# Performance work log

Hardware: AMD Instinct MI355X
Metric: run time of the kernel (lower is better)

The kernel has to match this reference:

```python
import jax, jax.numpy as jnp
import numpy as np

B, C, D, H, W_, CT = 2, 64, 12, 20, 40, 32


def setup_inputs() -> dict:
    key = jax.random.key(0)
    ks = jax.random.split(key, 8)
    def w(k, o, i):
        return jax.random.normal(k, (o, i), jnp.float32) / np.float32(np.sqrt(i))
    return dict(
        x=jax.random.normal(ks[0], (B, C, D, H, W_), jnp.float32),
        preds=jax.random.normal(ks[1], (B, D, H, W_), jnp.float32),
        Wq1=w(ks[2], CT, C), Wq2=w(ks[3], CT, CT),
        Wk1=w(ks[4], CT, C), Wk2=w(ks[5], CT, CT),
        Wv=w(ks[6], CT, C), Wo=w(ks[7], C, CT),
    )


def conv_bn_relu(x, Wm, eps=1e-5):
    # 1x1x1 Conv3d (no bias) + BatchNorm3d (batch stats, no affine) + ReLU
    y = jnp.einsum('bcdhw,oc->bodhw', x, Wm)
    mu = y.mean(axis=(0, 2, 3, 4), keepdims=True)
    var = y.var(axis=(0, 2, 3, 4), keepdims=True)
    return jax.nn.relu((y - mu) * jax.lax.rsqrt(var + eps))


def semantic_gather(x, preds):
    # Vectorized equivalent of the nested batch/disp-class loops:
    # per-pixel argmax over disparity planes, softmax within each argmax group,
    # scatter weighted feature into a dense (b, hw, d, c) tensor (zeros elsewhere).
    b, c, d, h, w = x.shape
    p = jax.nn.softmax(preds, axis=1).reshape(b, d, h * w).transpose(0, 2, 1)  # (b,hw,d)
    f = x.reshape(b, c, d, h * w).transpose(0, 3, 2, 1)                        # (b,hw,d,c)
    a = jnp.argmax(p, axis=-1)                                                 # (b,hw) segment ids
    pv = jnp.take_along_axis(p, a[..., None], axis=-1)[..., 0]                 # (b,hw) gathered prob

    def seg_softmax(vals, segs):
        # softmax over pixels sharing the same argmax disparity class
        m = jax.lax.stop_gradient(jax.ops.segment_max(vals, segs, num_segments=d))
        e = jnp.exp(vals - m[segs])
        s = jax.ops.segment_sum(e, segs, num_segments=d)
        return e / s[segs]

    wt = jax.vmap(seg_softmax)(pv, a)                                          # (b,hw)
    fg = jnp.take_along_axis(f, a[:, :, None, None], axis=2)[:, :, 0, :]       # (b,hw,c)
    oh = jax.nn.one_hot(a, d, dtype=x.dtype)                                   # (b,hw,d)
    feats_sl = oh[..., None] * (fg * wt[..., None])[:, :, None, :]             # (b,hw,d,c)
    return feats_sl.reshape(b, h, w, d, c).transpose(0, 4, 3, 1, 2)            # (b,c,d,h,w)


def reference(x, preds, Wq1, Wq2, Wk1, Wk2, Wv, Wo):
    feats_sl = semantic_gather(x, preds)
    key_feats = feats_sl + x
    # SelfAttentionBlock: query/key = 2 conv-bn-relu, value/out = 1 conv-bn-relu
    q = conv_bn_relu(conv_bn_relu(x, Wq1), Wq2)
    k = conv_bn_relu(conv_bn_relu(key_feats, Wk1), Wk2)
    v = conv_bn_relu(key_feats, Wv)
    b, ct, d, h, w = q.shape
    n = d * h * w
    qf = q.reshape(b, ct, n).transpose(0, 2, 1)   # (b,n,ct)
    kf = k.reshape(b, ct, n)                      # (b,ct,n)
    vf = v.reshape(b, ct, n).transpose(0, 2, 1)   # (b,n,ct)
    sim = jnp.einsum('bnc,bcm->bnm', qf, kf) * (ct ** -0.5)
    sim = jax.nn.softmax(sim, axis=-1)
    ctx = jnp.einsum('bnm,bmc->bnc', sim, vf).transpose(0, 2, 1).reshape(b, ct, d, h, w)
    return conv_bn_relu(ctx, Wo)
```

## Files before the change

kernel.cpp:

```cpp
#include <hip/hip_runtime.h>

#define NB 2
#define CIN 64
#define DD 12
#define HWP 800
#define NPOS 9600
#define CT 32
#define QKSCALE 0.25506601f
#define CSH 11.541560327f

typedef __attribute__((ext_vector_type(8))) short short8;
typedef __attribute__((ext_vector_type(16))) float f32x16;

__device__ __forceinline__ ushort f2bf(float x){
    union { float f; unsigned u; } v; v.f = x;
    unsigned r = v.u + 0x7fffu + ((v.u >> 16) & 1u);
    return (ushort)(r >> 16);
}

__global__ __launch_bounds__(256) void seg_kernel(const float* __restrict__ preds,
                                                  int* __restrict__ a, float* __restrict__ wt)
{
    int b = blockIdx.x / DD, seg = blockIdx.x % DD;
    __shared__ float lpv[HWP];
    __shared__ int   la[HWP];
    __shared__ float red[256];
    int t = threadIdx.x;
    for (int i=t; i<HWP; i+=256){
        const float* p = preds + (size_t)b*DD*HWP + i;
        float mx = -INFINITY; int am = 0;
        #pragma unroll
        for (int d=0; d<DD; ++d){ float v = p[d*HWP]; if (v > mx){ mx=v; am=d; } }
        float s = 0.f;
        #pragma unroll
        for (int d=0; d<DD; ++d) s += __expf(p[d*HWP]-mx);
        lpv[i] = 1.f/s; la[i] = am;
        if (seg == 0) a[b*HWP+i] = am;
    }
    __syncthreads();
    float mx = -INFINITY;
    for (int i=t; i<HWP; i+=256) if (la[i]==seg) mx = fmaxf(mx, lpv[i]);
    red[t]=mx; __syncthreads();
    for (int s=128; s>0; s>>=1){ if (t<s) red[t]=fmaxf(red[t],red[t+s]); __syncthreads(); }
    float m = red[0]; __syncthreads();
    if (m == -INFINITY) return;
    float sm = 0.f;
    for (int i=t; i<HWP; i+=256) if (la[i]==seg) sm += __expf(lpv[i]-m);
    red[t]=sm; __syncthreads();
    for (int s=128; s>0; s>>=1){ if (t<s) red[t]+=red[t+s]; __syncthreads(); }
    float ssum = red[0];
    for (int i=t; i<HWP; i+=256) if (la[i]==seg) wt[b*HWP+i] = __expf(lpv[i]-m)/ssum;
}

__global__ __launch_bounds__(256) void conv1_kernel(const float* __restrict__ x,
    const int* __restrict__ a, const float* __restrict__ wt,
    const float* __restrict__ Wq1, const float* __restrict__ Wk1, const float* __restrict__ Wv,
    float* __restrict__ q1, float* __restrict__ k1, float* __restrict__ v1,
    float* __restrict__ part)
{
    __shared__ float lw[6144];
    for (int i=threadIdx.x; i<2048; i+=256){ lw[i]=Wq1[i]; lw[2048+i]=Wk1[i]; lw[4096+i]=Wv[i]; }
    __syncthreads();
    int t = threadIdx.x;
    int posIdx = blockIdx.x*32 + (t&31);
    int g = t>>5;
    int b = posIdx / NPOS, pos = posIdx % NPOS;
    int d = pos / HWP, pix = pos % HWP;
    float fac = 1.f;
    if (a[b*HWP+pix] == d) fac += wt[b*HWP+pix];
    float acc[12];
    #pragma unroll
    for (int j=0;j<12;++j) acc[j]=0.f;
    const float* xb = x + (size_t)b*CIN*NPOS + pos;
    int chBase = g*12;
    for (int c=0;c<CIN;++c){
        float xv = xb[(size_t)c*NPOS];
        const float* wrow = &lw[chBase*64 + c];
        #pragma unroll
        for (int j=0;j<12;++j) acc[j] += xv * wrow[j*64];
    }
    #pragma unroll
    for (int j=0;j<12;++j){
        int ch = chBase + j;
        float val = acc[j];
        if (ch >= 32) val *= fac;
        acc[j] = val;
        if (ch < 32)       q1[((size_t)b*CT + ch)*NPOS + pos] = val;
        else if (ch < 64)  k1[((size_t)b*CT + (ch-32))*NPOS + pos] = val;
        else               v1[((size_t)b*CT + (ch-64))*NPOS + pos] = val;
    }
    #pragma unroll
    for (int j=0;j<12;++j){
        float s = acc[j], qs = acc[j]*acc[j];
        #pragma unroll
        for (int off=16; off; off>>=1){ s += __shfl_xor(s,off); qs += __shfl_xor(qs,off); }
        if ((t&31)==0){
            int ch = chBase+j;
            part[((size_t)ch*600 + blockIdx.x)*2]   = s;
            part[((size_t)ch*600 + blockIdx.x)*2+1] = qs;
        }
    }
}

__global__ __launch_bounds__(64) void statsfin_kernel(const float* __restrict__ part,
    float* __restrict__ mu, float* __restrict__ rs, int nblk)
{
    int ch = blockIdx.x;
    float s=0.f, q=0.f;
    for (int i=threadIdx.x; i<nblk; i+=64){
        s += part[((size_t)ch*nblk+i)*2];
        q += part[((size_t)ch*nblk+i)*2+1];
    }
    #pragma unroll
    for (int off=32; off; off>>=1){ s += __shfl_xor(s,off); q += __shfl_xor(q,off); }
    if (threadIdx.x==0){
        float m = s/19200.f;
        mu[ch]=m; rs[ch]=rsqrtf(q/19200.f - m*m + 1e-5f);
    }
}

__global__ __launch_bounds__(256) void conv2_kernel(const float* __restrict__ q1, const float* __restrict__ k1,
    const float* __restrict__ Wq2, const float* __restrict__ Wk2,
    const float* __restrict__ mu1, const float* __restrict__ rs1,
    float* __restrict__ q2, float* __restrict__ k2, float* __restrict__ part)
{
    __shared__ float lw[2048];
    for (int i=threadIdx.x; i<1024; i+=256){ lw[i]=Wq2[i]; lw[1024+i]=Wk2[i]; }
    __syncthreads();
    int t = threadIdx.x;
    int posIdx = blockIdx.x*32 + (t&31);
    int g = t>>5;
    int b = posIdx / NPOS, pos = posIdx % NPOS;
    const float* src = (g<4) ? q1 : k1;
    const float* wb  = (g<4) ? lw : (lw+1024);
    float* dst       = (g<4) ? q2 : k2;
    int so = (g<4) ? 0 : 32;
    int chBase = (g&3)*8;
    float acc[8];
    #pragma unroll
    for (int j=0;j<8;++j) acc[j]=0.f;
    for (int c=0;c<32;++c){
        float v = src[((size_t)b*CT + c)*NPOS + pos];
        float vn = fmaxf((v - mu1[so+c])*rs1[so+c], 0.f);
        const float* wrow = &wb[chBase*32 + c];
        #pragma unroll
        for (int j=0;j<8;++j) acc[j] += vn * wrow[j*32];
    }
    #pragma unroll
    for (int j=0;j<8;++j)
        dst[((size_t)b*CT + chBase + j)*NPOS + pos] = acc[j];
    #pragma unroll
    for (int j=0;j<8;++j){
        float s = acc[j], qs = acc[j]*acc[j];
        #pragma unroll
        for (int off=16; off; off>>=1){ s += __shfl_xor(s,off); qs += __shfl_xor(qs,off); }
        if ((t&31)==0){
            int ch = so + chBase + j;
            part[((size_t)ch*600 + blockIdx.x)*2]   = s;
            part[((size_t)ch*600 + blockIdx.x)*2+1] = qs;
        }
    }
}

__global__ __launch_bounds__(256) void pack_kernel(const float* __restrict__ q2, const float* __restrict__ k2,
    const float* __restrict__ v1,
    const float* __restrict__ mu2, const float* __restrict__ rs2,
    const float* __restrict__ muv, const float* __restrict__ rsv,
    ushort* __restrict__ Qbf, ushort* __restrict__ KP, ushort* __restrict__ VP)
{
    if (blockIdx.x < 75){
        int idx = blockIdx.x*256 + threadIdx.x;
        int b = idx / NPOS, pos = idx - b*NPOS;
        const float* qsrc = q2 + (size_t)b*CT*NPOS + pos;
        const float* ksrc = k2 + (size_t)b*CT*NPOS + pos;
        unsigned qw[16], kw[16];
        #pragma unroll
        for (int c2=0; c2<16; ++c2){
            int c0 = 2*c2, c1 = 2*c2+1;
            float a0 = fmaxf((qsrc[(size_t)c0*NPOS] - mu2[c0])*rs2[c0], 0.f)*QKSCALE;
            float a1 = fmaxf((qsrc[(size_t)c1*NPOS] - mu2[c1])*rs2[c1], 0.f)*QKSCALE;
            qw[c2] = (unsigned)f2bf(a0) | ((unsigned)f2bf(a1)<<16);
            float b0 = fmaxf((ksrc[(size_t)c0*NPOS] - mu2[32+c0])*rs2[32+c0], 0.f);
            float b1 = fmaxf((ksrc[(size_t)c1*NPOS] - mu2[32+c1])*rs2[32+c1], 0.f);
            kw[c2] = (unsigned)f2bf(b0) | ((unsigned)f2bf(b1)<<16);
        }
        uint4* qd = (uint4*)(Qbf + (size_t)idx*CT);
        #pragma unroll
        for (int j=0;j<4;++j)
            qd[j] = make_uint4(qw[4*j], qw[4*j+1], qw[4*j+2], qw[4*j+3]);
        int kb = pos >> 5, c = pos & 31;
        ushort* base = KP + ((size_t)(b*300 + kb))*1024;
        *(uint4*)(base + (c)*8)          = make_uint4(kw[0],kw[1],kw[2],kw[3]);
        *(uint4*)(base + (c+32)*8)       = make_uint4(kw[4],kw[5],kw[6],kw[7]);
        *(uint4*)(base + 512 + (c)*8)    = make_uint4(kw[8],kw[9],kw[10],kw[11]);
        *(uint4*)(base + 512 + (c+32)*8) = make_uint4(kw[12],kw[13],kw[14],kw[15]);
    } else {
        int idx = (blockIdx.x-75)*256 + threadIdx.x;
        int b = idx / 38400;
        int r = idx - b*38400;
        int c = r / 1200;
        int g8 = r - c*1200;
        int key = g8*8;
        int kb = g8 >> 2, q8 = g8 & 3;
        int p = q8 >> 1, hh = q8 & 1;
        const float* vs = v1 + ((size_t)b*CT + c)*NPOS + key;
        float m = muv[c], rr = rsv[c];
        unsigned wds[4];
        #pragma unroll
        for (int j=0;j<4;++j){
            float a0 = fmaxf((vs[2*j]   - m)*rr, 0.f);
            float a1 = fmaxf((vs[2*j+1] - m)*rr, 0.f);
            wds[j] = (unsigned)f2bf(a0) | ((unsigned)f2bf(a1)<<16);
        }
        *(uint4*)(VP + ((size_t)(b*300 + kb))*1024 + p*512 + (c + 32*hh)*8)
            = make_uint4(wds[0],wds[1],wds[2],wds[3]);
    }
}

__global__ __launch_bounds__(256) void attn_kernel(const ushort* __restrict__ Qbf,
    const ushort* __restrict__ KP, const ushort* __restrict__ VP,
    float* __restrict__ pacc, float* __restrict__ plsum)
{
    __shared__ float mrg[3][64][34];
    int blk = blockIdx.x;
    int b = blk / 450;
    int u = blk - b*450;
    int qb = u % 150, third = u / 150;
    int q0 = qb*64;
    int t = threadIdx.x, wv = t>>6, l = t&63;
    int c = l & 31, h = l >> 5;

    const char* QbU = (const char*)(Qbf + (size_t)b*NPOS*CT);
    const char* KPb = (const char*)KP;
    const char* VPb = (const char*)VP;

    union U { uint4 u; short8 s; };
    U qf0, qf1, qf2, qf3;
    qf0.u = *(const uint4*)(QbU + (((q0 + c)*CT + 8*h)<<1));
    qf1.u = *(const uint4*)(QbU + (((q0 + c)*CT + 16 + 8*h)<<1));
    qf2.u = *(const uint4*)(QbU + (((q0 + 32 + c)*CT + 8*h)<<1));
    qf3.u = *(const uint4*)(QbU + (((q0 + 32 + c)*CT + 16 + 8*h)<<1));

    U ones; ones.u = make_uint4(0x3F803F80u,0x3F803F80u,0x3F803F80u,0x3F803F80u);

    f32x16 acc0, acc1, accl0, accl1, cinit;
    #pragma unroll
    for (int r=0;r<16;++r){ acc0[r]=0.f; acc1[r]=0.f; accl0[r]=0.f; accl1[r]=0.f; cinit[r]=-CSH; }

    unsigned voff = (unsigned)(l*16);
    unsigned ko = (unsigned)(b*300 + third*100 + wv*25)*2048u;

    U nk0,nk1,nv0,nv1;
    nk0.u = *(const uint4*)(KPb + ko + voff);
    nk1.u = *(const uint4*)(KPb + ko + voff + 1024);
    nv0.u = *(const uint4*)(VPb + ko + voff);
    nv1.u = *(const uint4*)(VPb + ko + voff + 1024);

    for (int ck=0; ck<25; ++ck){
        U ka0=nk0, ka1=nk1, va0=nv0, va1=nv1;
        ko += (ck<24) ? 2048u : 0u;
        nk0.u = *(const uint4*)(KPb + ko + voff);
        nk1.u = *(const uint4*)(KPb + ko + voff + 1024);
        nv0.u = *(const uint4*)(VPb + ko + voff);
        nv1.u = *(const uint4*)(VPb + ko + voff + 1024);

        {
            f32x16 s = __builtin_amdgcn_mfma_f32_32x32x16_bf16(ka0.s, qf0.s, cinit,0,0,0);
            s = __builtin_amdgcn_mfma_f32_32x32x16_bf16(ka1.s, qf1.s, s, 0,0,0);
            float p[16];
            #pragma unroll
            for (int r=0;r<16;++r) asm("v_exp_f32 %0, %1" : "=v"(p[r]) : "v"(s[r]));
            unsigned E0,E1,E2,E3,E4,E5,E6,E7;
            asm("v_cvt_pk_bf16_f32 %0,%1,%2" : "=v"(E0) : "v"(p[0]),  "v"(p[1]));
            asm("v_cvt_pk_bf16_f32 %0,%1,%2" : "=v"(E1) : "v"(p[2]),  "v"(p[3]));
            asm("v_cvt_pk_bf16_f32 %0,%1,%2" : "=v"(E2) : "v"(p[4]),  "v"(p[5]));
            asm("v_cvt_pk_bf16_f32 %0,%1,%2" : "=v"(E3) : "v"(p[6]),  "v"(p[7]));
            asm("v_cvt_pk_bf16_f32 %0,%1,%2" : "=v"(E4) : "v"(p[8]),  "v"(p[9]));
            asm("v_cvt_pk_bf16_f32 %0,%1,%2" : "=v"(E5) : "v"(p[10]), "v"(p[11]));
            asm("v_cvt_pk_bf16_f32 %0,%1,%2" : "=v"(E6) : "v"(p[12]), "v"(p[13]));
            asm("v_cvt_pk_bf16_f32 %0,%1,%2" : "=v"(E7) : "v"(p[14]), "v"(p[15]));
            asm("v_permlane32_swap_b32 %0, %1" : "+v"(E0), "+v"(E2));
            asm("v_permlane32_swap_b32 %0, %1" : "+v"(E1), "+v"(E3));
            asm("v_permlane32_swap_b32 %0, %1" : "+v"(E4), "+v"(E6));
            asm("v_permlane32_swap_b32 %0, %1" : "+v"(E5), "+v"(E7));
            U pf1, pf2;
            pf1.u = make_uint4(E0,E1,E2,E3);
            pf2.u = make_uint4(E4,E5,E6,E7);
            acc0  = __builtin_amdgcn_mfma_f32_32x32x16_bf16(va0.s,  pf1.s, acc0, 0,0,0);
            accl0 = __builtin_amdgcn_mfma_f32_32x32x16_bf16(ones.s, pf1.s, accl0,0,0,0);
            acc0  = __builtin_amdgcn_mfma_f32_32x32x16_bf16(va1.s,  pf2.s, acc0, 0,0,0);
            accl0 = __builtin_amdgcn_mfma_f32_32x32x16_bf16(ones.s, pf2.s, accl0,0,0,0);
        }
        {
            f32x16 s = __builtin_amdgcn_mfma_f32_32x32x16_bf16(ka0.s, qf2.s, cinit,0,0,0);
            s = __builtin_amdgcn_mfma_f32_32x32x16_bf16(ka1.s, qf3.s, s, 0,0,0);
            float p[16];
            #pragma unroll
            for (int r=0;r<16;++r) asm("v_exp_f32 %0, %1" : "=v"(p[r]) : "v"(s[r]));
            unsigned E0,E1,E2,E3,E4,E5,E6,E7;
            asm("v_cvt_pk_bf16_f32 %0,%1,%2" : "=v"(E0) : "v"(p[0]),  "v"(p[1]));
            asm("v_cvt_pk_bf16_f32 %0,%1,%2" : "=v"(E1) : "v"(p[2]),  "v"(p[3]));
            asm("v_cvt_pk_bf16_f32 %0,%1,%2" : "=v"(E2) : "v"(p[4]),  "v"(p[5]));
            asm("v_cvt_pk_bf16_f32 %0,%1,%2" : "=v"(E3) : "v"(p[6]),  "v"(p[7]));
            asm("v_cvt_pk_bf16_f32 %0,%1,%2" : "=v"(E4) : "v"(p[8]),  "v"(p[9]));
            asm("v_cvt_pk_bf16_f32 %0,%1,%2" : "=v"(E5) : "v"(p[10]), "v"(p[11]));
            asm("v_cvt_pk_bf16_f32 %0,%1,%2" : "=v"(E6) : "v"(p[12]), "v"(p[13]));
            asm("v_cvt_pk_bf16_f32 %0,%1,%2" : "=v"(E7) : "v"(p[14]), "v"(p[15]));
            asm("v_permlane32_swap_b32 %0, %1" : "+v"(E0), "+v"(E2));
            asm("v_permlane32_swap_b32 %0, %1" : "+v"(E1), "+v"(E3));
            asm("v_permlane32_swap_b32 %0, %1" : "+v"(E4), "+v"(E6));
            asm("v_permlane32_swap_b32 %0, %1" : "+v"(E5), "+v"(E7));
            U pf1, pf2;
            pf1.u = make_uint4(E0,E1,E2,E3);
            pf2.u = make_uint4(E4,E5,E6,E7);
            acc1  = __builtin_amdgcn_mfma_f32_32x32x16_bf16(va0.s,  pf1.s, acc1, 0,0,0);
            accl1 = __builtin_amdgcn_mfma_f32_32x32x16_bf16(ones.s, pf1.s, accl1,0,0,0);
            acc1  = __builtin_amdgcn_mfma_f32_32x32x16_bf16(va1.s,  pf2.s, acc1, 0,0,0);
            accl1 = __builtin_amdgcn_mfma_f32_32x32x16_bf16(ones.s, pf2.s, accl1,0,0,0);
        }
    }

    float lsum0 = accl0[0];
    float lsum1 = accl1[0];

    if (wv > 0){
        float* mb = &mrg[wv-1][l][0];
        #pragma unroll
        for (int r=0;r<16;++r){ mb[r] = acc0[r]; mb[16+r] = acc1[r]; }
        mb[32] = lsum0; mb[33] = lsum1;
    }
    __syncthreads();
    if (wv == 0){
        #pragma unroll
        for (int w2=0; w2<3; ++w2){
            const float* mb = &mrg[w2][l][0];
            #pragma unroll
            for (int r=0;r<16;++r){ acc0[r] += mb[r]; acc1[r] += mb[16+r]; }
            lsum0 += mb[32]; lsum1 += mb[33];
        }
        float* pa = pacc + (size_t)(b*3 + third)*CT*NPOS;
        int pos0 = q0 + c, pos1 = q0 + 32 + c;
        #pragma unroll
        for (int r=0;r<16;++r){
            int rw = (r&3) + 8*(r>>2) + 4*h;
            pa[(size_t)rw*NPOS + pos0] = acc0[r];
            pa[(size_t)rw*NPOS + pos1] = acc1[r];
        }
        if (h == 0){
            plsum[(size_t)(b*3+third)*NPOS + pos0] = lsum0;
            plsum[(size_t)(b*3+third)*NPOS + pos1] = lsum1;
        }
    }
}

__global__ __launch_bounds__(256) void convo_kernel(const float* __restrict__ pacc,
    const float* __restrict__ plsum, const float* __restrict__ Wo,
    float* __restrict__ outraw, float* __restrict__ part)
{
    __shared__ float lw[2048];
    for (int i=threadIdx.x; i<2048; i+=256) lw[i]=Wo[i];
    __syncthreads();
    int t = threadIdx.x;
    int posIdx = blockIdx.x*32 + (t&31);
    int g = t>>5;
    int b = posIdx / NPOS, pos = posIdx % NPOS;
    const float* pA = pacc + (size_t)(b*3)*CT*NPOS + pos;
    const float* pB = pacc + (size_t)(b*3+1)*CT*NPOS + pos;
    const float* pC = pacc + (size_t)(b*3+2)*CT*NPOS + pos;
    float inv = 1.f/(plsum[(size_t)(b*3)*NPOS + pos] + plsum[(size_t)(b*3+1)*NPOS + pos]
                   + plsum[(size_t)(b*3+2)*NPOS + pos]);
    int chBase = g*8;
    float acc[8];
    #pragma unroll
    for (int j=0;j<8;++j) acc[j]=0.f;
    for (int c=0;c<32;++c){
        float v = (pA[(size_t)c*NPOS] + pB[(size_t)c*NPOS] + pC[(size_t)c*NPOS]) * inv;
        const float* wrow = &lw[chBase*32 + c];
        #pragma unroll
        for (int j=0;j<8;++j) acc[j] += v * wrow[j*32];
    }
    #pragma unroll
    for (int j=0;j<8;++j)
        outraw[((size_t)b*64 + chBase + j)*NPOS + pos] = acc[j];
    #pragma unroll
    for (int j=0;j<8;++j){
        float s = acc[j], qs = acc[j]*acc[j];
        #pragma unroll
        for (int off=16; off; off>>=1){ s += __shfl_xor(s,off); qs += __shfl_xor(qs,off); }
        if ((t&31)==0){
            int ch = chBase+j;
            part[((size_t)ch*600 + blockIdx.x)*2]   = s;
            part[((size_t)ch*600 + blockIdx.x)*2+1] = qs;
        }
    }
}

__global__ __launch_bounds__(256) void bn_relu_kernel(const float* __restrict__ src,
    const float* __restrict__ mu, const float* __restrict__ rs,
    float* __restrict__ dst, int C, int total)
{
    int idx = blockIdx.x*256 + threadIdx.x;
    if (idx >= total) return;
    int ch = (idx / NPOS) % C;
    dst[idx] = fmaxf((src[idx]-mu[ch])*rs[ch], 0.f);
}

extern "C" void kernel_launch(void* const* d_in, const int* in_sizes, int n_in,
                              void* d_out, int out_size, void* d_ws, size_t ws_size,
                              hipStream_t stream)
{
    const float* x     = (const float*)d_in[0];
    const float* preds = (const float*)d_in[1];
    const float* Wq1   = (const float*)d_in[2];
    const float* Wq2   = (const float*)d_in[3];
    const float* Wk1   = (const float*)d_in[4];
    const float* Wk2   = (const float*)d_in[5];
    const float* Wv    = (const float*)d_in[6];
    const float* Wo    = (const float*)d_in[7];
    float* out = (float*)d_out;

    float* w     = (float*)d_ws;
    int*   a_idx = (int*)d_ws;
    float* wt    = w + 4096;
    float* mu1   = w + 6656;
    float* rs1   = w + 6752;
    float* mu2   = w + 6848;
    float* rs2   = w + 6912;
    float* muo   = w + 6976;
    float* rso   = w + 7040;
    float* q1    = w + 8192;
    float* k1    = w + 622592;
    float* v1    = w + 1236992;
    float* q2    = w + 1851392;
    float* k2    = w + 2465792;
    ushort* Qbf  = (ushort*)(w + 8192);
    ushort* KP   = (ushort*)(w + 315392);
    ushort* VP   = (ushort*)(w + 3080192);
    float* pacc  = w + 622592;
    float* plsum = w + 3387392;
    float* part1 = w + 3444992;
    float* part2 = w + 3560192;
    float* parto = w + 3444992;

    seg_kernel  <<<24,  256,0,stream>>>(preds, a_idx, wt);
    conv1_kernel<<<600, 256,0,stream>>>(x, a_idx, wt, Wq1, Wk1, Wv, q1, k1, v1, part1);
    statsfin_kernel<<<96, 64,0,stream>>>(part1, mu1, rs1, 600);
    conv2_kernel<<<600, 256,0,stream>>>(q1, k1, Wq2, Wk2, mu1, rs1, q2, k2, part2);
    statsfin_kernel<<<64, 64,0,stream>>>(part2, mu2, rs2, 600);
    pack_kernel <<<375, 256,0,stream>>>(q2, k2, v1, mu2, rs2, mu1+64, rs1+64, Qbf, KP, VP);
    attn_kernel <<<900, 256,0,stream>>>(Qbf, KP, VP, pacc, plsum);
    convo_kernel<<<600, 256,0,stream>>>(pacc, plsum, Wo, out, parto);
    statsfin_kernel<<<64, 64,0,stream>>>(parto, muo, rso, 600);
    bn_relu_kernel<<<4800,256,0,stream>>>(out, muo, rso, out, 64, 1228800);
}
```

Measured before the change: 112.5 us.

## Split conv kernels across output-channel halves and raise MFMA wave priority in attention

The three pointwise conv kernels (conv1, conv2, convo) now launch twice as many blocks. Each block handles half of the output channels, with fewer accumulators per thread and a smaller shared weight tile, which gives more parallelism across the GPU's compute units for these small grids. In exchange, every input element is read twice from global memory. Separately, the attention kernel wraps its MFMA groups in s_setprio(1)/s_setprio(0) so waves issuing matrix ops get scheduling priority over waves doing exp and convert work.

```diff
diff --git a/kernel.cpp b/kernel.cpp
--- a/kernel.cpp
+++ b/kernel.cpp
@@ -58,30 +58,34 @@
     float* __restrict__ q1, float* __restrict__ k1, float* __restrict__ v1,
     float* __restrict__ part)
 {
-    __shared__ float lw[6144];
-    for (int i=threadIdx.x; i<2048; i+=256){ lw[i]=Wq1[i]; lw[2048+i]=Wk1[i]; lw[4096+i]=Wv[i]; }
+    __shared__ float lw[3072];
+    int cb = blockIdx.x / 600, blk = blockIdx.x - cb*600;
+    for (int i=threadIdx.x; i<3072; i+=256){
+        int gch = cb*48 + (i>>6), c = i&63;
+        lw[i] = (gch<32) ? Wq1[gch*64+c] : (gch<64) ? Wk1[(gch-32)*64+c] : Wv[(gch-64)*64+c];
+    }
     __syncthreads();
     int t = threadIdx.x;
-    int posIdx = blockIdx.x*32 + (t&31);
+    int posIdx = blk*32 + (t&31);
     int g = t>>5;
     int b = posIdx / NPOS, pos = posIdx % NPOS;
     int d = pos / HWP, pix = pos % HWP;
     float fac = 1.f;
     if (a[b*HWP+pix] == d) fac += wt[b*HWP+pix];
-    float acc[12];
-    #pragma unroll
-    for (int j=0;j<12;++j) acc[j]=0.f;
+    float acc[6];
+    #pragma unroll
+    for (int j=0;j<6;++j) acc[j]=0.f;
     const float* xb = x + (size_t)b*CIN*NPOS + pos;
-    int chBase = g*12;
+    int lBase = g*6;
     for (int c=0;c<CIN;++c){
         float xv = xb[(size_t)c*NPOS];
-        const float* wrow = &lw[chBase*64 + c];
-        #pragma unroll
-        for (int j=0;j<12;++j) acc[j] += xv * wrow[j*64];
-    }
-    #pragma unroll
-    for (int j=0;j<12;++j){
-        int ch = chBase + j;
+        const float* wrow = &lw[lBase*64 + c];
+        #pragma unroll
+        for (int j=0;j<6;++j) acc[j] += xv * wrow[j*64];
+    }
+    #pragma unroll
+    for (int j=0;j<6;++j){
+        int ch = cb*48 + lBase + j;
         float val = acc[j];
         if (ch >= 32) val *= fac;
         acc[j] = val;
@@ -90,14 +94,14 @@
         else               v1[((size_t)b*CT + (ch-64))*NPOS + pos] = val;
     }
     #pragma unroll
-    for (int j=0;j<12;++j){
+    for (int j=0;j<6;++j){
         float s = acc[j], qs = acc[j]*acc[j];
         #pragma unroll
         for (int off=16; off; off>>=1){ s += __shfl_xor(s,off); qs += __shfl_xor(qs,off); }
         if ((t&31)==0){
-            int ch = chBase+j;
-            part[((size_t)ch*600 + blockIdx.x)*2]   = s;
-            part[((size_t)ch*600 + blockIdx.x)*2+1] = qs;
+            int ch = cb*48 + lBase + j;
+            part[((size_t)ch*600 + blk)*2]   = s;
+            part[((size_t)ch*600 + blk)*2+1] = qs;
         }
     }
 }
@@ -124,40 +128,40 @@
     const float* __restrict__ mu1, const float* __restrict__ rs1,
     float* __restrict__ q2, float* __restrict__ k2, float* __restrict__ part)
 {
-    __shared__ float lw[2048];
-    for (int i=threadIdx.x; i<1024; i+=256){ lw[i]=Wq2[i]; lw[1024+i]=Wk2[i]; }
+    __shared__ float lw[1024];
+    int cb = blockIdx.x / 600, blk = blockIdx.x - cb*600;
+    for (int i=threadIdx.x; i<1024; i+=256) lw[i] = cb ? Wk2[i] : Wq2[i];
     __syncthreads();
     int t = threadIdx.x;
-    int posIdx = blockIdx.x*32 + (t&31);
+    int posIdx = blk*32 + (t&31);
     int g = t>>5;
     int b = posIdx / NPOS, pos = posIdx % NPOS;
-    const float* src = (g<4) ? q1 : k1;
-    const float* wb  = (g<4) ? lw : (lw+1024);
-    float* dst       = (g<4) ? q2 : k2;
-    int so = (g<4) ? 0 : 32;
-    int chBase = (g&3)*8;
-    float acc[8];
-    #pragma unroll
-    for (int j=0;j<8;++j) acc[j]=0.f;
+    const float* src = cb ? k1 : q1;
+    float* dst       = cb ? k2 : q2;
+    int so = cb*32;
+    int chBase = g*4;
+    float acc[4];
+    #pragma unroll
+    for (int j=0;j<4;++j) acc[j]=0.f;
     for (int c=0;c<32;++c){
         float v = src[((size_t)b*CT + c)*NPOS + pos];
         float vn = fmaxf((v - mu1[so+c])*rs1[so+c], 0.f);
-        const float* wrow = &wb[chBase*32 + c];
-        #pragma unroll
-        for (int j=0;j<8;++j) acc[j] += vn * wrow[j*32];
-    }
-    #pragma unroll
-    for (int j=0;j<8;++j)
+        const float* wrow = &lw[chBase*32 + c];
+        #pragma unroll
+        for (int j=0;j<4;++j) acc[j] += vn * wrow[j*32];
+    }
+    #pragma unroll
+    for (int j=0;j<4;++j)
         dst[((size_t)b*CT + chBase + j)*NPOS + pos] = acc[j];
     #pragma unroll
-    for (int j=0;j<8;++j){
+    for (int j=0;j<4;++j){
         float s = acc[j], qs = acc[j]*acc[j];
         #pragma unroll
         for (int off=16; off; off>>=1){ s += __shfl_xor(s,off); qs += __shfl_xor(qs,off); }
         if ((t&31)==0){
             int ch = so + chBase + j;
-            part[((size_t)ch*600 + blockIdx.x)*2]   = s;
-            part[((size_t)ch*600 + blockIdx.x)*2+1] = qs;
+            part[((size_t)ch*600 + blk)*2]   = s;
+            part[((size_t)ch*600 + blk)*2+1] = qs;
         }
     }
 }
@@ -265,8 +269,10 @@
         nv1.u = *(const uint4*)(VPb + ko + voff + 1024);
 
         {
+            __builtin_amdgcn_s_setprio(1);
             f32x16 s = __builtin_amdgcn_mfma_f32_32x32x16_bf16(ka0.s, qf0.s, cinit,0,0,0);
             s = __builtin_amdgcn_mfma_f32_32x32x16_bf16(ka1.s, qf1.s, s, 0,0,0);
+            __builtin_amdgcn_s_setprio(0);
             float p[16];
             #pragma unroll
             for (int r=0;r<16;++r) asm("v_exp_f32 %0, %1" : "=v"(p[r]) : "v"(s[r]));
@@ -286,14 +292,18 @@
             U pf1, pf2;
             pf1.u = make_uint4(E0,E1,E2,E3);
             pf2.u = make_uint4(E4,E5,E6,E7);
+            __builtin_amdgcn_s_setprio(1);
             acc0  = __builtin_amdgcn_mfma_f32_32x32x16_bf16(va0.s,  pf1.s, acc0, 0,0,0);
             accl0 = __builtin_amdgcn_mfma_f32_32x32x16_bf16(ones.s, pf1.s, accl0,0,0,0);
             acc0  = __builtin_amdgcn_mfma_f32_32x32x16_bf16(va1.s,  pf2.s, acc0, 0,0,0);
             accl0 = __builtin_amdgcn_mfma_f32_32x32x16_bf16(ones.s, pf2.s, accl0,0,0,0);
+            __builtin_amdgcn_s_setprio(0);
         }
         {
+            __builtin_amdgcn_s_setprio(1);
             f32x16 s = __builtin_amdgcn_mfma_f32_32x32x16_bf16(ka0.s, qf2.s, cinit,0,0,0);
             s = __builtin_amdgcn_mfma_f32_32x32x16_bf16(ka1.s, qf3.s, s, 0,0,0);
+            __builtin_amdgcn_s_setprio(0);
             float p[16];
             #pragma unroll
             for (int r=0;r<16;++r) asm("v_exp_f32 %0, %1" : "=v"(p[r]) : "v"(s[r]));
@@ -313,10 +323,12 @@
             U pf1, pf2;
             pf1.u = make_uint4(E0,E1,E2,E3);
             pf2.u = make_uint4(E4,E5,E6,E7);
+            __builtin_amdgcn_s_setprio(1);
             acc1  = __builtin_amdgcn_mfma_f32_32x32x16_bf16(va0.s,  pf1.s, acc1, 0,0,0);
             accl1 = __builtin_amdgcn_mfma_f32_32x32x16_bf16(ones.s, pf1.s, accl1,0,0,0);
             acc1  = __builtin_amdgcn_mfma_f32_32x32x16_bf16(va1.s,  pf2.s, acc1, 0,0,0);
             accl1 = __builtin_amdgcn_mfma_f32_32x32x16_bf16(ones.s, pf2.s, accl1,0,0,0);
+            __builtin_amdgcn_s_setprio(0);
         }
     }
 
@@ -357,11 +369,12 @@
     const float* __restrict__ plsum, const float* __restrict__ Wo,
     float* __restrict__ outraw, float* __restrict__ part)
 {
-    __shared__ float lw[2048];
-    for (int i=threadIdx.x; i<2048; i+=256) lw[i]=Wo[i];
+    __shared__ float lw[1024];
+    int cb = blockIdx.x / 600, blk = blockIdx.x - cb*600;
+    for (int i=threadIdx.x; i<1024; i+=256) lw[i] = Wo[cb*1024 + i];
     __syncthreads();
     int t = threadIdx.x;
-    int posIdx = blockIdx.x*32 + (t&31);
+    int posIdx = blk*32 + (t&31);
     int g = t>>5;
     int b = posIdx / NPOS, pos = posIdx % NPOS;
     const float* pA = pacc + (size_t)(b*3)*CT*NPOS + pos;
@@ -369,28 +382,28 @@
     const float* pC = pacc + (size_t)(b*3+2)*CT*NPOS + pos;
     float inv = 1.f/(plsum[(size_t)(b*3)*NPOS + pos] + plsum[(size_t)(b*3+1)*NPOS + pos]
                    + plsum[(size_t)(b*3+2)*NPOS + pos]);
-    int chBase = g*8;
-    float acc[8];
-    #pragma unroll
-    for (int j=0;j<8;++j) acc[j]=0.f;
+    int chBase = g*4;
+    float acc[4];
+    #pragma unroll
+    for (int j=0;j<4;++j) acc[j]=0.f;
     for (int c=0;c<32;++c){
         float v = (pA[(size_t)c*NPOS] + pB[(size_t)c*NPOS] + pC[(size_t)c*NPOS]) * inv;
         const float* wrow = &lw[chBase*32 + c];
         #pragma unroll
-        for (int j=0;j<8;++j) acc[j] += v * wrow[j*32];
-    }
-    #pragma unroll
-    for (int j=0;j<8;++j)
-        outraw[((size_t)b*64 + chBase + j)*NPOS + pos] = acc[j];
-    #pragma unroll
-    for (int j=0;j<8;++j){
+        for (int j=0;j<4;++j) acc[j] += v * wrow[j*32];
+    }
+    #pragma unroll
+    for (int j=0;j<4;++j)
+        outraw[((size_t)b*64 + cb*32 + chBase + j)*NPOS + pos] = acc[j];
+    #pragma unroll
+    for (int j=0;j<4;++j){
         float s = acc[j], qs = acc[j]*acc[j];
         #pragma unroll
         for (int off=16; off; off>>=1){ s += __shfl_xor(s,off); qs += __shfl_xor(qs,off); }
         if ((t&31)==0){
-            int ch = chBase+j;
-            part[((size_t)ch*600 + blockIdx.x)*2]   = s;
-            part[((size_t)ch*600 + blockIdx.x)*2+1] = qs;
+            int ch = cb*32 + chBase + j;
+            part[((size_t)ch*600 + blk)*2]   = s;
+            part[((size_t)ch*600 + blk)*2+1] = qs;
         }
     }
 }
@@ -443,13 +456,13 @@
     float* parto = w + 3444992;
 
     seg_kernel  <<<24,  256,0,stream>>>(preds, a_idx, wt);
-    conv1_kernel<<<600, 256,0,stream>>>(x, a_idx, wt, Wq1, Wk1, Wv, q1, k1, v1, part1);
+    conv1_kernel<<<1200,256,0,stream>>>(x, a_idx, wt, Wq1, Wk1, Wv, q1, k1, v1, part1);
     statsfin_kernel<<<96, 64,0,stream>>>(part1, mu1, rs1, 600);
-    conv2_kernel<<<600, 256,0,stream>>>(q1, k1, Wq2, Wk2, mu1, rs1, q2, k2, part2);
+    conv2_kernel<<<1200,256,0,stream>>>(q1, k1, Wq2, Wk2, mu1, rs1, q2, k2, part2);
     statsfin_kernel<<<64, 64,0,stream>>>(part2, mu2, rs2, 600);
     pack_kernel <<<375, 256,0,stream>>>(q2, k2, v1, mu2, rs2, mu1+64, rs1+64, Qbf, KP, VP);
     attn_kernel <<<900, 256,0,stream>>>(Qbf, KP, VP, pacc, plsum);
-    convo_kernel<<<600, 256,0,stream>>>(pacc, plsum, Wo, out, parto);
+    convo_kernel<<<1200,256,0,stream>>>(pacc, plsum, Wo, out, parto);
     statsfin_kernel<<<64, 64,0,stream>>>(parto, muo, rso, 600);
     bn_relu_kernel<<<4800,256,0,stream>>>(out, muo, rso, out, 64, 1228800);
 }
```

Result: no change. 114.6 us (+1.9%).
